# Performance work log

Measured on AMD Instinct MI355X. Metric: run time of the kernel, lower is better.

Reference implementation:

```python
import jax, jax.numpy as jnp
import numpy as np
import math

B, S, D, H = 2, 2048, 1024, 16
DK = D // H


def setup_inputs() -> dict:
    key = jax.random.key(0)
    ks = jax.random.split(key, 12)
    std = 1.0 / math.sqrt(D)
    inp = {
        "query": jax.random.normal(ks[0], (B, S, D), jnp.float32),
        "key": jax.random.normal(ks[1], (B, S, D), jnp.float32),
        "value": jax.random.normal(ks[2], (B, S, D), jnp.float32),
        # causal mask, broadcast over batch and heads
        "mask": jnp.tril(jnp.ones((S, S), jnp.int32))[None, None, :, :],
        # nn.Linear weights are [out_features, in_features]
        "Wq": jax.random.uniform(ks[3], (D, D), jnp.float32, -std, std),
        "bq": jax.random.uniform(ks[4], (D,), jnp.float32, -std, std),
        "Wk": jax.random.uniform(ks[5], (D, D), jnp.float32, -std, std),
        "bk": jax.random.uniform(ks[6], (D,), jnp.float32, -std, std),
        "Wv": jax.random.uniform(ks[7], (D, D), jnp.float32, -std, std),
        "bv": jax.random.uniform(ks[8], (D,), jnp.float32, -std, std),
        "Wo": jax.random.uniform(ks[9], (D, D), jnp.float32, -std, std),
        "bo": jax.random.uniform(ks[10], (D,), jnp.float32, -std, std),
    }
    return inp


def reference(query, key, value, mask, Wq, bq, Wk, bk, Wv, bv, Wo, bo):
    q = query @ Wq.T + bq  # [B,S,D]
    k = key @ Wk.T + bk
    v = value @ Wv.T + bv
    # Faithful to the original: a raw view (reshape), NOT a head-transpose split.
    q = q.reshape(B, H, S, DK)
    k = k.reshape(B, H, S, DK)
    v = v.reshape(B, H, S, DK)
    scores = jnp.einsum("bhqd,bhkd->bhqk", q, k) / math.sqrt(DK)
    scores = jnp.where(mask == 0, jnp.float32(-1e9), scores)
    weights = jax.nn.softmax(scores, axis=-1)
    # dropout(p=0.1) is identity in eval mode
    context = jnp.einsum("bhqk,bhkd->bhqd", weights, v)
    context = context.transpose(0, 2, 1, 3).reshape(B, S, D)
    return context @ Wo.T + bo
```

## Files before the change

### kernel.cpp

```cpp
#include <hip/hip_runtime.h>
#include <hip/hip_bf16.h>

#define BB 2
#define SS 2048
#define DD 1024
#define HH 16
#define DKK 64

typedef __attribute__((ext_vector_type(4))) float  f32x4;
typedef __attribute__((ext_vector_type(8))) short  s16x8;
typedef __attribute__((ext_vector_type(4))) short  s16x4;
typedef __attribute__((ext_vector_type(4))) float  fvec4;

__device__ __forceinline__ short f2bs(float f) {
    union { __hip_bfloat16 b; short s; } u;
    u.b = __float2bfloat16(f);
    return u.s;
}

__device__ __forceinline__ void gload_lds16(const short* g, short* l) {
    __builtin_amdgcn_global_load_lds((const __attribute__((address_space(1))) void*)g,
                                     (__attribute__((address_space(3))) void*)l, 16, 0, 0);
}

__global__ __launch_bounds__(256) void cvt_all(
    const float* __restrict__ q,  const float* __restrict__ k,  const float* __restrict__ v,
    const float* __restrict__ wq, const float* __restrict__ wk, const float* __restrict__ wv,
    const float* __restrict__ wo,
    short* __restrict__ qo,  short* __restrict__ ko,  short* __restrict__ vo,
    short* __restrict__ wqo, short* __restrict__ wko, short* __restrict__ wvo,
    short* __restrict__ woo)
{
    const float* src; short* dst; int n;
    switch (blockIdx.y) {
        case 0: src = q;  dst = qo;  n = BB * SS * DD; break;
        case 1: src = k;  dst = ko;  n = BB * SS * DD; break;
        case 2: src = v;  dst = vo;  n = BB * SS * DD; break;
        case 3: src = wq; dst = wqo; n = DD * DD; break;
        case 4: src = wk; dst = wko; n = DD * DD; break;
        case 5: src = wv; dst = wvo; n = DD * DD; break;
        default: src = wo; dst = woo; n = DD * DD; break;
    }
    int i = (blockIdx.x * 256 + threadIdx.x) * 8;
    const int stride = gridDim.x * 256 * 8;
    for (; i < n; i += stride) {
        fvec4 a = *(const fvec4*)&src[i];
        fvec4 b = *(const fvec4*)&src[i + 4];
        s16x8 o;
        o[0] = f2bs(a[0]); o[1] = f2bs(a[1]); o[2] = f2bs(a[2]); o[3] = f2bs(a[3]);
        o[4] = f2bs(b[0]); o[5] = f2bs(b[1]); o[6] = f2bs(b[2]); o[7] = f2bs(b[3]);
        *(s16x8*)&dst[i] = o;
    }
}

template<int BN, int NXSH, bool OUTF32>
__global__ __launch_bounds__(256) void gemm_nt_v2(
    const short* __restrict__ A0, const short* __restrict__ A1, const short* __restrict__ A2,
    const short* __restrict__ B0, const short* __restrict__ B1, const short* __restrict__ B2,
    const float* __restrict__ c0, const float* __restrict__ c1, const float* __restrict__ c2,
    void* __restrict__ O0, void* __restrict__ O1, void* __restrict__ O2,
    float os0, float os1, float os2,
    int ppx, int NY, int KL, int N, int K)
{
    const int d   = blockIdx.x;
    const int xcd = d & 7;
    const int s   = d >> 3;
    const int x   = s & ((1 << NXSH) - 1);
    const int pl  = s >> NXSH;
    const int panel = xcd * ppx + pl;
    const int y   = panel % NY;
    const int z   = panel / NY;

    const short* A    = z == 0 ? A0 : (z == 1 ? A1 : A2);
    const short* Bw   = z == 0 ? B0 : (z == 1 ? B1 : B2);
    const float* bias = z == 0 ? c0 : (z == 1 ? c1 : c2);
    void* Cp          = z == 0 ? O0 : (z == 1 ? O1 : O2);
    const float oscale = z == 0 ? os0 : (z == 1 ? os1 : os2);

    __shared__ short As[128][64];
    __shared__ short Bs[BN][64];

    const int tid  = threadIdx.x;
    const int lane = tid & 63;
    const int wid  = tid >> 6;
    const int r16  = lane & 15;
    const int g    = lane >> 4;
    const int m0   = y * 128;
    const int n0   = x * BN;
    constexpr int MR = 4;
    constexpr int NR = BN / 32;
    const int wr   = (wid >> 1) * 64;
    const int wc   = (wid & 1) * (BN / 2);
    const int srow8 = lane >> 3;
    const int c8    = lane & 7;

    f32x4 acc[MR][NR];
#pragma unroll
    for (int mi = 0; mi < MR; ++mi)
#pragma unroll
        for (int ni = 0; ni < NR; ++ni) acc[mi][ni] = (f32x4){0.f, 0.f, 0.f, 0.f};

    const int csrc = (c8 ^ srow8) * 8;
    const int nk = KL >> 6;
#pragma unroll 1
    for (int kt = 0; kt < nk; ++kt) {
        const int k0 = kt * 64;
        if (kt) __syncthreads();
#pragma unroll
        for (int q = 0; q < 4; ++q) {
            const int r = wid * 32 + q * 8 + srow8;
            gload_lds16(&A[(size_t)(m0 + r) * K + k0 + csrc], &As[wid * 32 + q * 8][0]);
        }
#pragma unroll
        for (int q = 0; q < BN / 32; ++q) {
            const int r = wid * (BN / 4) + q * 8 + srow8;
            gload_lds16(&Bw[(size_t)(n0 + r) * K + k0 + csrc], &Bs[wid * (BN / 4) + q * 8][0]);
        }
        __syncthreads();

#pragma unroll
        for (int kk = 0; kk < 2; ++kk) {
            s16x8 af[MR], bf[NR];
#pragma unroll
            for (int mi = 0; mi < MR; ++mi) {
                const int row = wr + mi * 16 + r16;
                af[mi] = *(const s16x8*)&As[row][((kk * 4 + g) ^ (row & 7)) * 8];
            }
#pragma unroll
            for (int ni = 0; ni < NR; ++ni) {
                const int row = wc + ni * 16 + r16;
                bf[ni] = *(const s16x8*)&Bs[row][((kk * 4 + g) ^ (row & 7)) * 8];
            }
#pragma unroll
            for (int mi = 0; mi < MR; ++mi)
#pragma unroll
                for (int ni = 0; ni < NR; ++ni)
                    acc[mi][ni] = __builtin_amdgcn_mfma_f32_16x16x32_bf16(
                        af[mi], bf[ni], acc[mi][ni], 0, 0, 0);
        }
    }

#pragma unroll
    for (int ni = 0; ni < NR; ++ni) {
        const int col = n0 + wc + ni * 16 + r16;
        const float bv = bias ? bias[col] : 0.f;
#pragma unroll
        for (int mi = 0; mi < MR; ++mi) {
#pragma unroll
            for (int r = 0; r < 4; ++r) {
                const int row = m0 + wr + mi * 16 + g * 4 + r;
                const float vv = (acc[mi][ni][r] + bv) * oscale;
                if constexpr (OUTF32)
                    ((float*)Cp)[(size_t)row * N + col] = vv;
                else
                    ((short*)Cp)[(size_t)row * N + col] = f2bs(vv);
            }
        }
    }
}

__global__ __launch_bounds__(256) void mha_transpose_v(
    const short* __restrict__ vp, short* __restrict__ vT)
{
    const int st = blockIdx.x;
    const int bh = blockIdx.y;
    const short* src = vp + (size_t)bh * SS * DKK;
    short*       dst = vT + (size_t)bh * SS * DKK;
    const int tid = threadIdx.x;
#pragma unroll
    for (int i = 0; i < 2; ++i) {
        const int c  = tid + i * 256;
        const int dk = c >> 3;
        const int sc = c & 7;
        const int s0 = st * 64 + sc * 8;
        s16x8 v;
#pragma unroll
        for (int j = 0; j < 8; ++j) v[j] = src[(size_t)(s0 + j) * DKK + dk];
        *(s16x8*)&dst[(size_t)dk * SS + s0] = v;
    }
}

__global__ __launch_bounds__(256, 2) void mha_attn(
    const short* __restrict__ qp, const short* __restrict__ kp,
    const short* __restrict__ vT, short* __restrict__ ctx)
{
    __shared__ short Ks[2][64][64];
    __shared__ short Vs[2][64][64];
    __shared__ short P[4][16][72];

    const int tid  = threadIdx.x;
    const int wid  = tid >> 6;
    const int lane = tid & 63;
    const int r16  = lane & 15;
    const int g    = lane >> 4;

    const int bh  = blockIdx.x;
    const int bxp = blockIdx.y;
    const int b   = bh >> 4;
    const int h   = bh & 15;

    const short* Qh = qp + (size_t)bh * SS * DKK;
    const short* Kh = kp + (size_t)bh * SS * DKK;
    const short* Vh = vT + (size_t)bh * SS * DKK;

    const int srow = lane >> 3;
    const int csw  = (((lane & 7) ^ srow) & 7) * 8;
    const int r0   = wid * 16;

    auto STAGE = [&](int buf, int j) {
        const int k0 = j * 64;
        const int rA = r0 + srow;
        const int rB = rA + 8;
        gload_lds16(&Kh[(size_t)(k0 + rA) * DKK + csw], &Ks[buf][r0][0]);
        gload_lds16(&Kh[(size_t)(k0 + rB) * DKK + csw], &Ks[buf][r0 + 8][0]);
        gload_lds16(&Vh[(size_t)rA * SS + k0 + csw],    &Vs[buf][r0][0]);
        gload_lds16(&Vh[(size_t)rB * SS + k0 + csw],    &Vs[buf][r0 + 8][0]);
    };

#pragma unroll 1
    for (int t = 0; t < 2; ++t) {
        const int grp = t ? (31 - bxp) : bxp;
        const int qr0 = grp * 64 + wid * 16;
        const int nkt = grp + 1;

        const s16x8 qf0 = *(const s16x8*)&Qh[(size_t)(qr0 + r16) * DKK + g * 8];
        const s16x8 qf1 = *(const s16x8*)&Qh[(size_t)(qr0 + r16) * DKK + 32 + g * 8];

        f32x4 po[4];
#pragma unroll
        for (int i = 0; i < 4; ++i) po[i] = (f32x4){0.f, 0.f, 0.f, 0.f};
        float l_[4] = {0.f, 0.f, 0.f, 0.f};

        STAGE(0, 0);

#pragma unroll 1
        for (int j = 0; j < nkt; ++j) {
            const int cur = j & 1;
            const int k0 = j * 64;
            if (j + 1 < nkt) {
                STAGE(cur ^ 1, j + 1);
                asm volatile("s_waitcnt vmcnt(4)" ::: "memory");
            } else {
                asm volatile("s_waitcnt vmcnt(0)" ::: "memory");
            }
            __builtin_amdgcn_s_barrier();
            __builtin_amdgcn_sched_barrier(0);

            f32x4 sc[4];
            __builtin_amdgcn_s_setprio(1);
#pragma unroll
            for (int cg = 0; cg < 4; ++cg) {
                const int R  = cg * 16 + r16;
                const int sw = R & 7;
                const s16x8 kf0 = *(const s16x8*)&Ks[cur][R][((g ^ sw) & 7) * 8];
                const s16x8 kf1 = *(const s16x8*)&Ks[cur][R][(((4 + g) ^ sw) & 7) * 8];
                f32x4 tt = (f32x4){0.f, 0.f, 0.f, 0.f};
                tt = __builtin_amdgcn_mfma_f32_16x16x32_bf16(qf0, kf0, tt, 0, 0, 0);
                tt = __builtin_amdgcn_mfma_f32_16x16x32_bf16(qf1, kf1, tt, 0, 0, 0);
                sc[cg] = tt;
            }
            __builtin_amdgcn_s_setprio(0);

            if (j == nkt - 1) {
#pragma unroll
                for (int cg = 0; cg < 4; ++cg)
#pragma unroll
                    for (int r = 0; r < 4; ++r)
                        if (k0 + cg * 16 + r16 > qr0 + g * 4 + r) sc[cg][r] = -1e9f;
            }
#pragma unroll
            for (int cg = 0; cg < 4; ++cg)
#pragma unroll
                for (int r = 0; r < 4; ++r) {
                    const float p = __expf(sc[cg][r]);
                    l_[r] += p;
                    P[wid][g * 4 + r][cg * 16 + r16] = f2bs(p);
                }
            const s16x8 pf0 = *(const s16x8*)&P[wid][r16][g * 8];
            const s16x8 pf1 = *(const s16x8*)&P[wid][r16][32 + g * 8];

            __builtin_amdgcn_s_setprio(1);
#pragma unroll
            for (int dg = 0; dg < 4; ++dg) {
                const int Rv = dg * 16 + r16;
                const int sw = Rv & 7;
                const s16x8 vf0 = *(const s16x8*)&Vs[cur][Rv][((g ^ sw) & 7) * 8];
                const s16x8 vf1 = *(const s16x8*)&Vs[cur][Rv][(((4 + g) ^ sw) & 7) * 8];
                po[dg] = __builtin_amdgcn_mfma_f32_16x16x32_bf16(pf0, vf0, po[dg], 0, 0, 0);
                po[dg] = __builtin_amdgcn_mfma_f32_16x16x32_bf16(pf1, vf1, po[dg], 0, 0, 0);
            }
            __builtin_amdgcn_s_setprio(0);

            __builtin_amdgcn_sched_barrier(0);
            asm volatile("s_waitcnt lgkmcnt(0)" ::: "memory");
            __builtin_amdgcn_s_barrier();
        }

#pragma unroll
        for (int r = 0; r < 4; ++r) {
#pragma unroll
            for (int off = 1; off < 16; off <<= 1)
                l_[r] += __shfl_xor(l_[r], off);
        }
#pragma unroll
        for (int dg = 0; dg < 4; ++dg)
#pragma unroll
            for (int r = 0; r < 4; ++r) {
                const int srw = qr0 + g * 4 + r;
                const float v = po[dg][r] * __builtin_amdgcn_rcpf(l_[r]);
                ctx[((size_t)(b * SS + srw)) * DD + h * 64 + dg * 16 + r16] = f2bs(v);
            }
    }
}

extern "C" void kernel_launch(void* const* d_in, const int* in_sizes, int n_in,
                              void* d_out, int out_size, void* d_ws, size_t ws_size,
                              hipStream_t stream) {
    const float* query = (const float*)d_in[0];
    const float* key   = (const float*)d_in[1];
    const float* value = (const float*)d_in[2];
    const float* Wq = (const float*)d_in[4];
    const float* bq = (const float*)d_in[5];
    const float* Wk = (const float*)d_in[6];
    const float* bk = (const float*)d_in[7];
    const float* Wv = (const float*)d_in[8];
    const float* bv = (const float*)d_in[9];
    const float* Wo = (const float*)d_in[10];
    const float* bo = (const float*)d_in[11];
    float* out = (float*)d_out;

    const size_t elems = (size_t)BB * SS * DD;
    const size_t wel   = (size_t)DD * DD;
    short* qx  = (short*)d_ws;
    short* kx  = qx + elems;
    short* vx  = kx + elems;
    short* wqx = vx + elems;
    short* wkx = wqx + wel;
    short* wvx = wkx + wel;
    short* wox = wvx + wel;
    short* qp  = wox + wel;
    short* kp  = qp + elems;
    short* vp  = kp + elems;
    short* vT  = qx;
    short* ctx = vx;

    cvt_all<<<dim3(1024, 7), 256, 0, stream>>>(query, key, value, Wq, Wk, Wv, Wo,
                                               qx, kx, vx, wqx, wkx, wvx, wox);
    gemm_nt_v2<128, 3, false><<<dim3(768), 256, 0, stream>>>(
        qx, kx, vx, wqx, wkx, wvx, bq, bk, bv, qp, kp, vp,
        0.125f, 1.0f, 1.0f, 12, 32, 1024, DD, DD);
    mha_transpose_v<<<dim3(SS / 64, BB * HH), 256, 0, stream>>>(vp, vT);
    mha_attn<<<dim3(BB * HH, 16), 256, 0, stream>>>(qp, kp, vT, ctx);
    gemm_nt_v2<64, 4, true><<<dim3(512), 256, 0, stream>>>(
        ctx, ctx, ctx, wox, wox, wox, bo, bo, bo, out, out, out,
        1.0f, 1.0f, 1.0f, 4, 32, 1024, DD, DD);
}
```

Before: 121.2 us.

## Enlarge attention query tile to 128 rows per block with XCD-aware mapping

The attention kernel now gives each block a 128-row query tile, with each wave handling two 16-row sub-blocks. This replaces the two 64-row tiles per block of the old load-balanced pairing, so each K/V tile staged in LDS is reused by twice as many query rows. A linearised 1D grid maps blocks so that heads sharing K/V sit on the same XCD, and pairs mirrored tiles across the halves of the grid for causal balance. Waves whose rows lie wholly before the current key tile skip compute. The cost is more registers per wave and more wasted work on the causal diagonal, which now spans two key tiles.

```diff
diff --git a/kernel.cpp b/kernel.cpp
--- a/kernel.cpp
+++ b/kernel.cpp
@@ -186,7 +186,7 @@
 {
     __shared__ short Ks[2][64][64];
     __shared__ short Vs[2][64][64];
-    __shared__ short P[4][16][72];
+    __shared__ short P[4][32][72];
 
     const int tid  = threadIdx.x;
     const int wid  = tid >> 6;
@@ -194,10 +194,14 @@
     const int r16  = lane & 15;
     const int g    = lane >> 4;
 
-    const int bh  = blockIdx.x;
-    const int bxp = blockIdx.y;
-    const int b   = bh >> 4;
-    const int h   = bh & 15;
+    const int lin  = blockIdx.x;
+    const int xcd  = lin & 7;
+    const int bh   = (xcd << 2) | ((lin >> 3) & 3);
+    const int gg   = (lin >> 5) & 7;
+    const int half = (lin >> 8) & 1;
+    const int G    = half ? (15 - gg) : gg;
+    const int b    = bh >> 4;
+    const int h    = bh & 15;
 
     const short* Qh = qp + (size_t)bh * SS * DKK;
     const short* Kh = kp + (size_t)bh * SS * DKK;
@@ -217,36 +221,41 @@
         gload_lds16(&Vh[(size_t)rB * SS + k0 + csw],    &Vs[buf][r0 + 8][0]);
     };
 
+    const int qbase = G * 128;
+    const int wrow  = qbase + wid * 32;
+    const int nkt   = 2 * G + 2;
+
+    s16x8 qf[2][2];
+#pragma unroll
+    for (int rb = 0; rb < 2; ++rb)
+#pragma unroll
+        for (int hh = 0; hh < 2; ++hh)
+            qf[rb][hh] = *(const s16x8*)&Qh[(size_t)(wrow + rb * 16 + r16) * DKK + hh * 32 + g * 8];
+
+    f32x4 po[2][4];
+#pragma unroll
+    for (int rb = 0; rb < 2; ++rb)
+#pragma unroll
+        for (int i = 0; i < 4; ++i) po[rb][i] = (f32x4){0.f, 0.f, 0.f, 0.f};
+    float l_[2][4] = {{0.f, 0.f, 0.f, 0.f}, {0.f, 0.f, 0.f, 0.f}};
+
+    STAGE(0, 0);
+
 #pragma unroll 1
-    for (int t = 0; t < 2; ++t) {
-        const int grp = t ? (31 - bxp) : bxp;
-        const int qr0 = grp * 64 + wid * 16;
-        const int nkt = grp + 1;
-
-        const s16x8 qf0 = *(const s16x8*)&Qh[(size_t)(qr0 + r16) * DKK + g * 8];
-        const s16x8 qf1 = *(const s16x8*)&Qh[(size_t)(qr0 + r16) * DKK + 32 + g * 8];
-
-        f32x4 po[4];
-#pragma unroll
-        for (int i = 0; i < 4; ++i) po[i] = (f32x4){0.f, 0.f, 0.f, 0.f};
-        float l_[4] = {0.f, 0.f, 0.f, 0.f};
-
-        STAGE(0, 0);
-
-#pragma unroll 1
-        for (int j = 0; j < nkt; ++j) {
-            const int cur = j & 1;
-            const int k0 = j * 64;
-            if (j + 1 < nkt) {
-                STAGE(cur ^ 1, j + 1);
-                asm volatile("s_waitcnt vmcnt(4)" ::: "memory");
-            } else {
-                asm volatile("s_waitcnt vmcnt(0)" ::: "memory");
-            }
-            __builtin_amdgcn_s_barrier();
-            __builtin_amdgcn_sched_barrier(0);
-
-            f32x4 sc[4];
+    for (int j = 0; j < nkt; ++j) {
+        const int cur = j & 1;
+        const int k0 = j * 64;
+        if (j + 1 < nkt) {
+            STAGE(cur ^ 1, j + 1);
+            asm volatile("s_waitcnt vmcnt(4)" ::: "memory");
+        } else {
+            asm volatile("s_waitcnt vmcnt(0)" ::: "memory");
+        }
+        __builtin_amdgcn_s_barrier();
+        __builtin_amdgcn_sched_barrier(0);
+
+        if (k0 < wrow + 32) {
+            f32x4 sc[2][4];
             __builtin_amdgcn_s_setprio(1);
 #pragma unroll
             for (int cg = 0; cg < 4; ++cg) {
@@ -254,31 +263,42 @@
                 const int sw = R & 7;
                 const s16x8 kf0 = *(const s16x8*)&Ks[cur][R][((g ^ sw) & 7) * 8];
                 const s16x8 kf1 = *(const s16x8*)&Ks[cur][R][(((4 + g) ^ sw) & 7) * 8];
-                f32x4 tt = (f32x4){0.f, 0.f, 0.f, 0.f};
-                tt = __builtin_amdgcn_mfma_f32_16x16x32_bf16(qf0, kf0, tt, 0, 0, 0);
-                tt = __builtin_amdgcn_mfma_f32_16x16x32_bf16(qf1, kf1, tt, 0, 0, 0);
-                sc[cg] = tt;
+#pragma unroll
+                for (int rb = 0; rb < 2; ++rb) {
+                    f32x4 tt = (f32x4){0.f, 0.f, 0.f, 0.f};
+                    tt = __builtin_amdgcn_mfma_f32_16x16x32_bf16(qf[rb][0], kf0, tt, 0, 0, 0);
+                    tt = __builtin_amdgcn_mfma_f32_16x16x32_bf16(qf[rb][1], kf1, tt, 0, 0, 0);
+                    sc[rb][cg] = tt;
+                }
             }
             __builtin_amdgcn_s_setprio(0);
 
-            if (j == nkt - 1) {
+            if (j >= nkt - 2) {
+#pragma unroll
+                for (int rb = 0; rb < 2; ++rb)
+#pragma unroll
+                    for (int cg = 0; cg < 4; ++cg)
+#pragma unroll
+                        for (int r = 0; r < 4; ++r)
+                            if (k0 + cg * 16 + r16 > wrow + rb * 16 + g * 4 + r)
+                                sc[rb][cg][r] = -1e9f;
+            }
+#pragma unroll
+            for (int rb = 0; rb < 2; ++rb)
 #pragma unroll
                 for (int cg = 0; cg < 4; ++cg)
 #pragma unroll
-                    for (int r = 0; r < 4; ++r)
-                        if (k0 + cg * 16 + r16 > qr0 + g * 4 + r) sc[cg][r] = -1e9f;
-            }
-#pragma unroll
-            for (int cg = 0; cg < 4; ++cg)
-#pragma unroll
-                for (int r = 0; r < 4; ++r) {
-                    const float p = __expf(sc[cg][r]);
-                    l_[r] += p;
-                    P[wid][g * 4 + r][cg * 16 + r16] = f2bs(p);
-                }
-            const s16x8 pf0 = *(const s16x8*)&P[wid][r16][g * 8];
-            const s16x8 pf1 = *(const s16x8*)&P[wid][r16][32 + g * 8];
-
+                    for (int r = 0; r < 4; ++r) {
+                        const float p = __expf(sc[rb][cg][r]);
+                        l_[rb][r] += p;
+                        P[wid][rb * 16 + g * 4 + r][cg * 16 + r16] = f2bs(p);
+                    }
+            s16x8 pf[2][2];
+#pragma unroll
+            for (int rb = 0; rb < 2; ++rb) {
+                pf[rb][0] = *(const s16x8*)&P[wid][rb * 16 + r16][g * 8];
+                pf[rb][1] = *(const s16x8*)&P[wid][rb * 16 + r16][32 + g * 8];
+            }
             __builtin_amdgcn_s_setprio(1);
 #pragma unroll
             for (int dg = 0; dg < 4; ++dg) {
@@ -286,28 +306,34 @@
                 const int sw = Rv & 7;
                 const s16x8 vf0 = *(const s16x8*)&Vs[cur][Rv][((g ^ sw) & 7) * 8];
                 const s16x8 vf1 = *(const s16x8*)&Vs[cur][Rv][(((4 + g) ^ sw) & 7) * 8];
-                po[dg] = __builtin_amdgcn_mfma_f32_16x16x32_bf16(pf0, vf0, po[dg], 0, 0, 0);
-                po[dg] = __builtin_amdgcn_mfma_f32_16x16x32_bf16(pf1, vf1, po[dg], 0, 0, 0);
+#pragma unroll
+                for (int rb = 0; rb < 2; ++rb) {
+                    po[rb][dg] = __builtin_amdgcn_mfma_f32_16x16x32_bf16(pf[rb][0], vf0, po[rb][dg], 0, 0, 0);
+                    po[rb][dg] = __builtin_amdgcn_mfma_f32_16x16x32_bf16(pf[rb][1], vf1, po[rb][dg], 0, 0, 0);
+                }
             }
             __builtin_amdgcn_s_setprio(0);
-
-            __builtin_amdgcn_sched_barrier(0);
-            asm volatile("s_waitcnt lgkmcnt(0)" ::: "memory");
-            __builtin_amdgcn_s_barrier();
-        }
-
+        }
+
+        __builtin_amdgcn_sched_barrier(0);
+        asm volatile("s_waitcnt lgkmcnt(0)" ::: "memory");
+        __builtin_amdgcn_s_barrier();
+    }
+
+#pragma unroll
+    for (int rb = 0; rb < 2; ++rb) {
 #pragma unroll
         for (int r = 0; r < 4; ++r) {
 #pragma unroll
             for (int off = 1; off < 16; off <<= 1)
-                l_[r] += __shfl_xor(l_[r], off);
+                l_[rb][r] += __shfl_xor(l_[rb][r], off);
         }
 #pragma unroll
         for (int dg = 0; dg < 4; ++dg)
 #pragma unroll
             for (int r = 0; r < 4; ++r) {
-                const int srw = qr0 + g * 4 + r;
-                const float v = po[dg][r] * __builtin_amdgcn_rcpf(l_[r]);
+                const int srw = wrow + rb * 16 + g * 4 + r;
+                const float v = po[rb][dg][r] * __builtin_amdgcn_rcpf(l_[rb][r]);
                 ctx[((size_t)(b * SS + srw)) * DD + h * 64 + dg * 16 + r16] = f2bs(v);
             }
     }
@@ -350,7 +376,7 @@
         qx, kx, vx, wqx, wkx, wvx, bq, bk, bv, qp, kp, vp,
         0.125f, 1.0f, 1.0f, 12, 32, 1024, DD, DD);
     mha_transpose_v<<<dim3(SS / 64, BB * HH), 256, 0, stream>>>(vp, vT);
-    mha_attn<<<dim3(BB * HH, 16), 256, 0, stream>>>(qp, kp, vT, ctx);
+    mha_attn<<<dim3(512), 256, 0, stream>>>(qp, kp, vT, ctx);
     gemm_nt_v2<64, 4, true><<<dim3(512), 256, 0, stream>>>(
         ctx, ctx, ctx, wox, wox, wox, bo, bo, bo, out, out, out,
         1.0f, 1.0f, 1.0f, 4, 32, 1024, DD, DD);
```

New measurement: 127.8 us. 1.05x slower.

## Transpose score MFMA to pack P stores, drop K/V double buffering

Applied to the files above, without the earlier changes.

Swaps the MFMA operand order so each lane holds four consecutive key columns for one query row. The probabilities can then be packed with v_cvt_pk_bf16_f32 and written to LDS as 8-byte stores instead of scalar 2-byte stores. The row sum becomes one scalar per lane, reduced with two shuffles instead of sixteen. It also removes the double-buffered async K/V prefetch in favour of a single buffer loaded between two __syncthreads, which exposes global load latency on every tile.

```diff
diff --git a/kernel.cpp b/kernel.cpp
--- a/kernel.cpp
+++ b/kernel.cpp
@@ -11,11 +11,18 @@
 typedef __attribute__((ext_vector_type(8))) short  s16x8;
 typedef __attribute__((ext_vector_type(4))) short  s16x4;
 typedef __attribute__((ext_vector_type(4))) float  fvec4;
+typedef __attribute__((ext_vector_type(2))) unsigned int u32x2;
 
 __device__ __forceinline__ short f2bs(float f) {
     union { __hip_bfloat16 b; short s; } u;
     u.b = __float2bfloat16(f);
     return u.s;
+}
+
+__device__ __forceinline__ unsigned cvtpk(float lo, float hi) {
+    unsigned r;
+    asm("v_cvt_pk_bf16_f32 %0, %1, %2" : "=v"(r) : "v"(lo), "v"(hi));
+    return r;
 }
 
 __device__ __forceinline__ void gload_lds16(const short* g, short* l) {
@@ -184,8 +191,8 @@
     const short* __restrict__ qp, const short* __restrict__ kp,
     const short* __restrict__ vT, short* __restrict__ ctx)
 {
-    __shared__ short Ks[2][64][64];
-    __shared__ short Vs[2][64][64];
+    __shared__ short Ks[64][64];
+    __shared__ short Vs[64][64];
     __shared__ short P[4][16][72];
 
     const int tid  = threadIdx.x;
@@ -207,16 +214,6 @@
     const int csw  = (((lane & 7) ^ srow) & 7) * 8;
     const int r0   = wid * 16;
 
-    auto STAGE = [&](int buf, int j) {
-        const int k0 = j * 64;
-        const int rA = r0 + srow;
-        const int rB = rA + 8;
-        gload_lds16(&Kh[(size_t)(k0 + rA) * DKK + csw], &Ks[buf][r0][0]);
-        gload_lds16(&Kh[(size_t)(k0 + rB) * DKK + csw], &Ks[buf][r0 + 8][0]);
-        gload_lds16(&Vh[(size_t)rA * SS + k0 + csw],    &Vs[buf][r0][0]);
-        gload_lds16(&Vh[(size_t)rB * SS + k0 + csw],    &Vs[buf][r0 + 8][0]);
-    };
-
 #pragma unroll 1
     for (int t = 0; t < 2; ++t) {
         const int grp = t ? (31 - bxp) : bxp;
@@ -229,22 +226,21 @@
         f32x4 po[4];
 #pragma unroll
         for (int i = 0; i < 4; ++i) po[i] = (f32x4){0.f, 0.f, 0.f, 0.f};
-        float l_[4] = {0.f, 0.f, 0.f, 0.f};
-
-        STAGE(0, 0);
+        float lsum = 0.f;
 
 #pragma unroll 1
         for (int j = 0; j < nkt; ++j) {
-            const int cur = j & 1;
             const int k0 = j * 64;
-            if (j + 1 < nkt) {
-                STAGE(cur ^ 1, j + 1);
-                asm volatile("s_waitcnt vmcnt(4)" ::: "memory");
-            } else {
-                asm volatile("s_waitcnt vmcnt(0)" ::: "memory");
-            }
-            __builtin_amdgcn_s_barrier();
-            __builtin_amdgcn_sched_barrier(0);
+            __syncthreads();
+            {
+                const int rowA = r0 + srow;
+                const int rowB = rowA + 8;
+                gload_lds16(&Kh[(size_t)(k0 + rowA) * DKK + csw], &Ks[r0][0]);
+                gload_lds16(&Kh[(size_t)(k0 + rowB) * DKK + csw], &Ks[r0 + 8][0]);
+                gload_lds16(&Vh[(size_t)rowA * SS + k0 + csw], &Vs[r0][0]);
+                gload_lds16(&Vh[(size_t)rowB * SS + k0 + csw], &Vs[r0 + 8][0]);
+            }
+            __syncthreads();
 
             f32x4 sc[4];
             __builtin_amdgcn_s_setprio(1);
@@ -252,11 +248,11 @@
             for (int cg = 0; cg < 4; ++cg) {
                 const int R  = cg * 16 + r16;
                 const int sw = R & 7;
-                const s16x8 kf0 = *(const s16x8*)&Ks[cur][R][((g ^ sw) & 7) * 8];
-                const s16x8 kf1 = *(const s16x8*)&Ks[cur][R][(((4 + g) ^ sw) & 7) * 8];
+                const s16x8 kf0 = *(const s16x8*)&Ks[R][((g ^ sw) & 7) * 8];
+                const s16x8 kf1 = *(const s16x8*)&Ks[R][(((4 + g) ^ sw) & 7) * 8];
                 f32x4 tt = (f32x4){0.f, 0.f, 0.f, 0.f};
-                tt = __builtin_amdgcn_mfma_f32_16x16x32_bf16(qf0, kf0, tt, 0, 0, 0);
-                tt = __builtin_amdgcn_mfma_f32_16x16x32_bf16(qf1, kf1, tt, 0, 0, 0);
+                tt = __builtin_amdgcn_mfma_f32_16x16x32_bf16(kf0, qf0, tt, 0, 0, 0);
+                tt = __builtin_amdgcn_mfma_f32_16x16x32_bf16(kf1, qf1, tt, 0, 0, 0);
                 sc[cg] = tt;
             }
             __builtin_amdgcn_s_setprio(0);
@@ -266,16 +262,20 @@
                 for (int cg = 0; cg < 4; ++cg)
 #pragma unroll
                     for (int r = 0; r < 4; ++r)
-                        if (k0 + cg * 16 + r16 > qr0 + g * 4 + r) sc[cg][r] = -1e9f;
-            }
-#pragma unroll
-            for (int cg = 0; cg < 4; ++cg)
-#pragma unroll
-                for (int r = 0; r < 4; ++r) {
-                    const float p = __expf(sc[cg][r]);
-                    l_[r] += p;
-                    P[wid][g * 4 + r][cg * 16 + r16] = f2bs(p);
-                }
+                        if (k0 + cg * 16 + g * 4 + r > qr0 + r16) sc[cg][r] = -1e9f;
+            }
+#pragma unroll
+            for (int cg = 0; cg < 4; ++cg) {
+                const float p0 = __expf(sc[cg][0]);
+                const float p1 = __expf(sc[cg][1]);
+                const float p2 = __expf(sc[cg][2]);
+                const float p3 = __expf(sc[cg][3]);
+                lsum += (p0 + p1) + (p2 + p3);
+                u32x2 w;
+                w[0] = cvtpk(p0, p1);
+                w[1] = cvtpk(p2, p3);
+                *(u32x2*)&P[wid][r16][cg * 16 + g * 4] = w;
+            }
             const s16x8 pf0 = *(const s16x8*)&P[wid][r16][g * 8];
             const s16x8 pf1 = *(const s16x8*)&P[wid][r16][32 + g * 8];
 
@@ -284,30 +284,27 @@
             for (int dg = 0; dg < 4; ++dg) {
                 const int Rv = dg * 16 + r16;
                 const int sw = Rv & 7;
-                const s16x8 vf0 = *(const s16x8*)&Vs[cur][Rv][((g ^ sw) & 7) * 8];
-                const s16x8 vf1 = *(const s16x8*)&Vs[cur][Rv][(((4 + g) ^ sw) & 7) * 8];
+                const s16x8 vf0 = *(const s16x8*)&Vs[Rv][((g ^ sw) & 7) * 8];
+                const s16x8 vf1 = *(const s16x8*)&Vs[Rv][(((4 + g) ^ sw) & 7) * 8];
                 po[dg] = __builtin_amdgcn_mfma_f32_16x16x32_bf16(pf0, vf0, po[dg], 0, 0, 0);
                 po[dg] = __builtin_amdgcn_mfma_f32_16x16x32_bf16(pf1, vf1, po[dg], 0, 0, 0);
             }
             __builtin_amdgcn_s_setprio(0);
-
-            __builtin_amdgcn_sched_barrier(0);
-            asm volatile("s_waitcnt lgkmcnt(0)" ::: "memory");
-            __builtin_amdgcn_s_barrier();
-        }
-
-#pragma unroll
-        for (int r = 0; r < 4; ++r) {
-#pragma unroll
-            for (int off = 1; off < 16; off <<= 1)
-                l_[r] += __shfl_xor(l_[r], off);
-        }
+        }
+
+        lsum += __shfl_xor(lsum, 16);
+        lsum += __shfl_xor(lsum, 32);
+        const float linv = __builtin_amdgcn_rcpf(lsum);
+        float rowinv[4];
+#pragma unroll
+        for (int r = 0; r < 4; ++r)
+            rowinv[r] = __shfl(linv, g * 4 + r);
 #pragma unroll
         for (int dg = 0; dg < 4; ++dg)
 #pragma unroll
             for (int r = 0; r < 4; ++r) {
                 const int srw = qr0 + g * 4 + r;
-                const float v = po[dg][r] * __builtin_amdgcn_rcpf(l_[r]);
+                const float v = po[dg][r] * rowinv[r];
                 ctx[((size_t)(b * SS + srw)) * DD + h * 64 + dg * 16 + r16] = f2bs(v);
             }
     }
```

Result: no change. 120.3 us (-0.7%).
